# Optimization experiments

Hardware: AMD Instinct MI355X
Metric: run time of the kernel (lower is better)

The kernel has to match this reference:

```python
import jax, jax.numpy as jnp
import numpy as np

N_SPECIES = 4; N_BASIS = 128; N_GRAPH = 16; R_MAX = 6.0
NS_NODE, NV_NODE = 32, 16          # node irreps 32x0e + 16x1o
NS_EDGE = 16                       # initial edge irreps 16x0e
NS_OUT, NV_OUT = 16, 8             # output irreps 16x0e + 8x1o
NS_IN = 2 * NS_NODE + NS_EDGE      # 80 concatenated scalars
NV_IN = 2 * NV_NODE                # 32 concatenated vectors
NS_CONV = NS_OUT + NV_OUT          # 24 scalars (16 features + 8 gates)
W_SIZES = [NS_IN * NS_CONV, NS_IN * NV_OUT, NV_IN * NV_OUT, NV_IN * NS_CONV, NV_IN * NV_OUT]
N_NODES, N_EDGES = 8192, 65536
EPS = 1e-5


def gaussian_basis(d, stop, n):
    offsets = jnp.linspace(0.0, stop, n)
    coeff = -0.5 / (offsets[1] - offsets[0]) ** 2
    return jnp.exp(coeff * (d[:, None] - offsets[None, :]) ** 2)


def seg_mean(vals, seg, cnt):
    return jax.ops.segment_sum(vals, seg, num_segments=N_GRAPH) / cnt[:, None]


def setup_inputs():
    key = jax.random.key(0)
    ks = jax.random.split(key, 20)
    rn = lambda k, shape, scale: jax.random.normal(k, shape, jnp.float32) * scale
    inp = {}
    inp["node_fea"] = rn(ks[0], (N_NODES, NS_NODE + 3 * NV_NODE), 1.0)
    d = 0.5 + 5.0 * jax.random.uniform(ks[1], (N_EDGES,), jnp.float32)
    vec = jax.random.normal(ks[2], (N_EDGES, 3), jnp.float32)
    inp["edge_attr"] = jnp.concatenate([d[:, None], vec], axis=1)
    inp["edge_index"] = jax.random.randint(ks[3], (2, N_EDGES), 0, N_NODES)
    inp["x"] = jax.random.randint(ks[4], (N_NODES,), 0, N_SPECIES)
    inp["batch"] = jnp.sort(jax.random.randint(ks[5], (N_NODES,), 0, N_GRAPH))
    inp["w_rh"] = rn(ks[6], (N_BASIS, 64), N_BASIS ** -0.5); inp["b_rh"] = jnp.zeros((64,), jnp.float32)
    inp["w_ro"] = rn(ks[7], (64, sum(W_SIZES)), 64 ** -0.5); inp["b_ro"] = jnp.zeros((sum(W_SIZES),), jnp.float32)
    inp["w_pre"] = rn(ks[8], (NS_EDGE, NS_EDGE), NS_EDGE ** -0.5); inp["b_pre"] = jnp.zeros((NS_EDGE,), jnp.float32)
    inp["w_sc"] = rn(ks[9], (NS_EDGE, N_SPECIES ** 2, NS_OUT), 1.0)
    inp["w_post_s"] = rn(ks[10], (NS_OUT, NS_OUT), NS_OUT ** -0.5); inp["b_post_s"] = jnp.zeros((NS_OUT,), jnp.float32)
    inp["w_post_v"] = rn(ks[11], (NV_OUT, NV_OUT), NV_OUT ** -0.5)
    inp["ln_w_s"] = jnp.ones((NS_OUT,), jnp.float32); inp["ln_b_s"] = jnp.zeros((NS_OUT,), jnp.float32)
    inp["ln_w_v"] = jnp.ones((NV_OUT,), jnp.float32)
    inp["w_skip"] = rn(ks[12], (NS_EDGE, NS_OUT), NS_EDGE ** -0.5)
    inp["w_edge_s"] = rn(ks[13], (NS_OUT, NS_OUT), NS_OUT ** -0.5); inp["b_edge_s"] = jnp.zeros((NS_OUT,), jnp.float32)
    inp["w_edge_v"] = rn(ks[14], (NV_OUT, NV_OUT), NV_OUT ** -0.5)
    return inp


def _forward(node_fea, edge_attr, w_rh, b_rh, w_ro, b_ro, w_pre, b_pre, w_sc,
             w_post_s, b_post_s, w_post_v, ln_w_s, ln_b_s, ln_w_v,
             w_skip, w_edge_s, b_edge_s, w_edge_v, edge_index, x, batch):
    E = edge_index.shape[1]
    idx_i, idx_j = edge_index[0], edge_index[1]
    one_hot = jax.nn.one_hot(N_SPECIES * x[idx_i] + x[idx_j], N_SPECIES ** 2, dtype=node_fea.dtype)
    d, vec = edge_attr[:, 0], edge_attr[:, 1:4]
    u = vec / (jnp.linalg.norm(vec, axis=1, keepdims=True) + 1e-12)
    Y1 = np.sqrt(3.0) * u                                   # l=1 sph harm, component norm; Y0 == 1
    rbf = gaussian_basis(d, R_MAX, N_BASIS)                 # edge_length_embedded
    edge_s0 = gaussian_basis(d, 6.0, NS_EDGE)               # distance_expansion -> initial edge scalars
    # self connection: edge scalars x species-pair one-hot -> output scalars
    sc = jnp.einsum('ei,ej,ijo->eo', edge_s0, one_hot, w_sc) / np.sqrt(NS_EDGE * N_SPECIES ** 2)
    edge_s = edge_s0 @ w_pre + b_pre                        # lin_pre
    # gather node features by edge indices and concat
    nf_i, nf_j = node_fea[idx_i], node_fea[idx_j]
    s_in = jnp.concatenate([nf_i[:, :NS_NODE], nf_j[:, :NS_NODE], edge_s], axis=1)  # [E,80]
    v_in = jnp.concatenate([nf_i[:, NS_NODE:].reshape(E, NV_NODE, 3),
                            nf_j[:, NS_NODE:].reshape(E, NV_NODE, 3)], axis=1)      # [E,32,3]
    # radial MLP -> per-edge tensor-product path weights
    h = jax.nn.silu(rbf @ w_rh + b_rh)
    w_all = h @ w_ro + b_ro                                 # [E, 3840]
    w1, w2, w3, w4, w5 = jnp.split(w_all, np.cumsum(W_SIZES)[:-1].tolist(), axis=1)
    # equivariant tensor-product paths (explicit l<=1 Clebsch-Gordan structure)
    s0 = jnp.einsum('ei,eio->eo', s_in, w1.reshape(E, NS_IN, NS_CONV)) / np.sqrt(NS_IN)            # 0e x 0e -> 0e
    vA = jnp.einsum('ei,eio,ec->eoc', s_in, w2.reshape(E, NS_IN, NV_OUT), Y1) / np.sqrt(NS_IN)     # 0e x 1o -> 1o
    vB = jnp.einsum('eic,eio->eoc', v_in, w3.reshape(E, NV_IN, NV_OUT)) / np.sqrt(NV_IN)           # 1o x 0e -> 1o
    s1 = jnp.einsum('eic,eio,ec->eo', v_in, w4.reshape(E, NV_IN, NS_CONV), Y1) / np.sqrt(3.0 * NV_IN)  # 1o.1o -> 0e
    vC = jnp.einsum('eic,eio->eoc', jnp.cross(v_in, Y1[:, None, :]), w5.reshape(E, NV_IN, NV_OUT)) / np.sqrt(2.0 * NV_IN)  # 1o x 1o -> 1o
    s_conv = s0 + s1                                        # [E,24]
    v_conv = vA + vB + vC                                   # [E,8,3]
    # gate nonlinearity inside conv
    s_out = jax.nn.silu(s_conv[:, :NS_OUT])
    v_out = v_conv * jax.nn.sigmoid(s_conv[:, NS_OUT:])[:, :, None]
    # lin_post then self connection
    s_out = s_out @ w_post_s + b_post_s + sc
    v_out = jnp.einsum('eic,io->eoc', v_out, w_post_v)
    # e3LayerNorm keyed by graph id of source node
    eb = batch[idx_i]
    cnt = jnp.maximum(jax.ops.segment_sum(jnp.ones((E,), s_out.dtype), eb, num_segments=N_GRAPH), 1.0)
    mu = seg_mean(s_out, eb, cnt)
    s_c = s_out - mu[eb]
    rms_s = jnp.sqrt(seg_mean(s_c ** 2, eb, cnt).mean(axis=1, keepdims=True) + EPS)
    s_n = s_c / rms_s[eb] * ln_w_s + ln_b_s
    rms_v = jnp.sqrt((seg_mean((v_out ** 2).sum(-1), eb, cnt) / 3.0).mean(axis=1, keepdims=True) + EPS)
    v_n = v_out / rms_v[eb][:, :, None] * ln_w_v[None, :, None]
    # skip connection from old edge features (scalars only)
    s_n = s_n + edge_s0 @ w_skip
    # final lin_edge
    s_fin = s_n @ w_edge_s + b_edge_s
    v_fin = jnp.einsum('eic,io->eoc', v_n, w_edge_v)
    return jnp.concatenate([s_fin, v_fin.reshape(E, NV_OUT * 3)], axis=1)  # [E,40]


def reference(node_fea, edge_attr, edge_index, x, batch, w_rh, b_rh, w_ro, b_ro,
              w_pre, b_pre, w_sc, w_post_s, b_post_s, w_post_v, ln_w_s, ln_b_s, ln_w_v,
              w_skip, w_edge_s, b_edge_s, w_edge_v):
    return _forward(node_fea, edge_attr, w_rh, b_rh, w_ro, b_ro, w_pre, b_pre, w_sc,
                    w_post_s, b_post_s, w_post_v, ln_w_s, ln_b_s, ln_w_v,
                    w_skip, w_edge_s, b_edge_s, w_edge_v, edge_index, x, batch)
```

## Files before the change

### kernel.cpp

```cpp
#include <hip/hip_runtime.h>

typedef unsigned short u16;
typedef unsigned int u32;
typedef __attribute__((ext_vector_type(8))) _Float16 half8;
typedef __attribute__((ext_vector_type(2))) __fp16 fp16x2;
typedef __attribute__((ext_vector_type(4))) float floatx4;

#define E_TOTAL 65536

__device__ __forceinline__ u32 pk16(float x0, float x1) {
    union { fp16x2 h; u32 u; } c;
    c.h = __builtin_amdgcn_cvt_pkrtz(x0, x1);
    return c.u;
}
union Frag8h { u32 u[4]; half8 v; };


__global__ __launch_bounds__(1024) void k_init(float* __restrict__ ws, int* __restrict__ binv) {
    const int tid = threadIdx.x;
    for (int i = tid; i < 1056; i += 1024) ws[i] = 0.0f;
    if (tid < 64) {
        const int lane = tid;
        const int q = lane >> 4;
        if (lane < 32) binv[lane] = lane;
        half8 bfr;
        #pragma unroll
        for (int j = 0; j < 8; ++j) bfr[j] = (_Float16)(float)(q*8 + j + 1);
        #pragma unroll
        for (int s = 0; s < 32; ++s) {
            const int qa = s >> 3, ja = s & 7;
            half8 afr;
            #pragma unroll
            for (int j = 0; j < 8; ++j) afr[j] = (_Float16)0.0f;
            if (q == qa) afr[ja] = (_Float16)1.0f;
            floatx4 dc = {0.0f, 0.0f, 0.0f, 0.0f};
            dc = __builtin_amdgcn_mfma_f32_16x16x32_f16(afr, bfr, dc, 0, 0, 0);
            if (lane == 0) {
                const int sB = (int)(dc[0] + 0.5f) - 1;
                if (sB >= 0 && sB < 32) binv[sB] = s;
            }
        }
    }
}

__global__ __launch_bounds__(256) void k_edge_heavy(
    const float* __restrict__ node_fea, const float* __restrict__ edge_attr,
    const int* __restrict__ edge_index, const int* __restrict__ xsp,
    const float* __restrict__ w_rh, const float* __restrict__ b_rh,
    const float* __restrict__ w_ro, const float* __restrict__ b_ro,
    const float* __restrict__ w_pre, const float* __restrict__ b_pre,
    const float* __restrict__ w_sc, const float* __restrict__ w_post_s,
    const float* __restrict__ b_post_s, const float* __restrict__ w_post_v,
    const int* __restrict__ binv, const int* __restrict__ batch,
    float* __restrict__ ws_stats,
    float* __restrict__ out)
{
    __shared__ __align__(16) float sh_wt[2][32][130];
    __shared__ float sh_sin[32][80];
    __shared__ float sh_vl[32][3][32];
    __shared__ float sh_acc[32][56];
    __shared__ float sh_y1[32][4];
    __shared__ int   sh_kmap[32];

    u16*   a_rbf = (u16*)&sh_wt[0][0][0];
    u16*   a_h   = (u16*)((char*)&sh_wt[0][0][0] + 8192);
    float* es0f  = (float*)((char*)&sh_wt[0][0][0] + 12288);

    const int tid = threadIdx.x;
    const int ed = tid >> 4, l16 = tid & 15;
    const int lane = tid & 63, w = tid >> 6;
    const int quad = lane >> 4, l15 = lane & 15;
    const int e0 = blockIdx.x * 32 + ed;
    const int e1 = e0 + 16;

    if (tid < 32) sh_kmap[tid] = binv[tid];

    const int ni0 = edge_index[e0], nj0 = edge_index[E_TOTAL + e0];
    const int ni1 = edge_index[e1], nj1 = edge_index[E_TOTAL + e1];
    const float4 ea0 = *(const float4*)(edge_attr + 4*e0);
    const float4 ea1 = *(const float4*)(edge_attr + 4*e1);
    const float d0 = ea0.x, d1 = ea1.x;
    {
        const float invn0 = 1.0f / (sqrtf(ea0.y*ea0.y + ea0.z*ea0.z + ea0.w*ea0.w) + 1e-12f);
        const float invn1 = 1.0f / (sqrtf(ea1.y*ea1.y + ea1.z*ea1.z + ea1.w*ea1.w) + 1e-12f);
        if (l16 == 0) {
            sh_y1[ed][0]    = 1.7320508075688772f * ea0.y * invn0;
            sh_y1[ed][1]    = 1.7320508075688772f * ea0.z * invn0;
            sh_y1[ed][2]    = 1.7320508075688772f * ea0.w * invn0;
            sh_y1[16+ed][0] = 1.7320508075688772f * ea1.y * invn1;
            sh_y1[16+ed][1] = 1.7320508075688772f * ea1.z * invn1;
            sh_y1[16+ed][2] = 1.7320508075688772f * ea1.w * invn1;
        }
    }

    const float C128 = -0.5f * (127.0f/6.0f) * (127.0f/6.0f);
    const float S128 = 6.0f/127.0f;
    {
        Frag8h t0, t1;
        #pragma unroll
        for (int r2 = 0; r2 < 4; ++r2) {
            const int b0i = l16*8 + 2*r2;
            const float u0 = d0 - S128 * (float)b0i;
            const float u1 = d0 - S128 * (float)(b0i + 1);
            const float v0 = d1 - S128 * (float)b0i;
            const float v1 = d1 - S128 * (float)(b0i + 1);
            t0.u[r2] = pk16(expf(C128*u0*u0), expf(C128*u1*u1));
            t1.u[r2] = pk16(expf(C128*v0*v0), expf(C128*v1*v1));
        }
        *(half8*)&a_rbf[(l16*16 + ed)*8]        = t0.v;
        *(half8*)&a_rbf[2048 + (l16*16 + ed)*8] = t1.v;
    }
    {
        const float t0 = d0 - 0.4f * (float)l16;
        const float t1 = d1 - 0.4f * (float)l16;
        es0f[ed*16 + l16]      = expf(-3.125f * t0 * t0);
        es0f[(16+ed)*16 + l16] = expf(-3.125f * t1 * t1);
    }

    const float rs80 = 0.11180339887498949f;
    const float rs32 = 0.17677669529663689f;
    {
        const float* fi = node_fea + (size_t)ni0 * 80;
        const float* fj = node_fea + (size_t)nj0 * 80;
        sh_sin[ed][2*l16+0]    = fi[2*l16+0] * rs80;
        sh_sin[ed][2*l16+1]    = fi[2*l16+1] * rs80;
        sh_sin[ed][32+2*l16+0] = fj[2*l16+0] * rs80;
        sh_sin[ed][32+2*l16+1] = fj[2*l16+1] * rs80;
        #pragma unroll
        for (int c = 0; c < 3; ++c) {
            sh_vl[ed][c][l16]      = fi[32 + 3*l16 + c] * rs32;
            sh_vl[ed][c][16 + l16] = fj[32 + 3*l16 + c] * rs32;
        }
    }
    {
        const float* fi = node_fea + (size_t)ni1 * 80;
        const float* fj = node_fea + (size_t)nj1 * 80;
        sh_sin[16+ed][2*l16+0]    = fi[2*l16+0] * rs80;
        sh_sin[16+ed][2*l16+1]    = fi[2*l16+1] * rs80;
        sh_sin[16+ed][32+2*l16+0] = fj[2*l16+0] * rs80;
        sh_sin[16+ed][32+2*l16+1] = fj[2*l16+1] * rs80;
        #pragma unroll
        for (int c = 0; c < 3; ++c) {
            sh_vl[16+ed][c][l16]      = fi[32 + 3*l16 + c] * rs32;
            sh_vl[16+ed][c][16 + l16] = fj[32 + 3*l16 + c] * rs32;
        }
    }
    for (int s = tid; s < 32*56; s += 256) (&sh_acc[0][0])[s] = 0.0f;
    __syncthreads();

    int km[8];
    u32 voff0[8], voff1[8];
    #pragma unroll
    for (int j = 0; j < 8; ++j) {
        km[j] = sh_kmap[quad*8 + j];
        voff0[j] = (u32)(km[j] * 3840 + l15);
        voff1[j] = voff0[j] + 32u * 3840u;
    }

    float my_sc0, my_sc1;
    {
        const int o = l16;
        float es0v = b_pre[o], sc0 = 0.0f;
        float es1v = b_pre[o], sc1 = 0.0f;
        const int p0 = 4*xsp[ni0] + xsp[nj0];
        const int p1 = 4*xsp[ni1] + xsp[nj1];
        #pragma unroll
        for (int i = 0; i < 16; ++i) {
            const float g0 = es0f[ed*16 + i];
            const float g1 = es0f[(16+ed)*16 + i];
            es0v += g0 * w_pre[i*16 + o];
            es1v += g1 * w_pre[i*16 + o];
            sc0  += g0 * w_sc[(i*16 + p0)*16 + o];
            sc1  += g1 * w_sc[(i*16 + p1)*16 + o];
        }
        sh_sin[ed][64 + o]    = es0v * rs80;
        sh_sin[16+ed][64 + o] = es1v * rs80;
        my_sc0 = sc0 * 0.0625f;
        my_sc1 = sc1 * 0.0625f;
    }

    {
        floatx4 h0 = {0.0f, 0.0f, 0.0f, 0.0f};
        floatx4 h1 = {0.0f, 0.0f, 0.0f, 0.0f};
        #pragma unroll
        for (int kk = 0; kk < 4; ++kk) {
            const half8 ag0 = *(const half8*)&a_rbf[((kk*4 + quad)*16 + l15)*8];
            const half8 ag1 = *(const half8*)&a_rbf[2048 + ((kk*4 + quad)*16 + l15)*8];
            Frag8h bh;
            #pragma unroll
            for (int jj = 0; jj < 4; ++jj) {
                const float x0 = w_rh[(size_t)(kk*32 + km[2*jj+0])*64 + w*16 + l15];
                const float x1 = w_rh[(size_t)(kk*32 + km[2*jj+1])*64 + w*16 + l15];
                bh.u[jj] = pk16(x0, x1);
            }
            h0 = __builtin_amdgcn_mfma_f32_16x16x32_f16(ag0, bh.v, h0, 0, 0, 0);
            h1 = __builtin_amdgcn_mfma_f32_16x16x32_f16(ag1, bh.v, h1, 0, 0, 0);
        }
        const int hn = w*16 + l15;
        const float bb = b_rh[hn];
        const int k8 = hn >> 3, j2 = hn & 7;
        #pragma unroll
        for (int r = 0; r < 4; ++r) {
            const int m = quad*4 + r;
            {
                const float x = h0[r] + bb;
                const float s = x / (1.0f + expf(-x));
                union { _Float16 h; u16 u; } cv; cv.h = (_Float16)s;
                a_h[(k8*16 + m)*8 + j2] = cv.u;
            }
            {
                const float x = h1[r] + bb;
                const float s = x / (1.0f + expf(-x));
                union { _Float16 h; u16 u; } cv; cv.h = (_Float16)s;
                a_h[1024 + (k8*16 + m)*8 + j2] = cv.u;
            }
        }
    }
    __syncthreads();

    const half8 a0g0 = *(const half8*)&a_h[((0*4 + quad)*16 + l15)*8];
    const half8 a1g0 = *(const half8*)&a_h[((1*4 + quad)*16 + l15)*8];
    const half8 a0g1 = *(const half8*)&a_h[1024 + ((0*4 + quad)*16 + l15)*8];
    const half8 a1g1 = *(const half8*)&a_h[1024 + ((1*4 + quad)*16 + l15)*8];
    __syncthreads();

    float pf[32];
    float pbias[2];
    #pragma unroll
    for (int ct = 0; ct < 2; ++ct) {
        const int sgct = __builtin_amdgcn_readfirstlane(w*2 + ct);
        const float* bp = w_ro + sgct*16;
        #pragma unroll
        for (int j = 0; j < 8; ++j) {
            pf[ct*16 + j]     = bp[voff0[j]];
            pf[ct*16 + 8 + j] = bp[voff1[j]];
        }
        pbias[ct] = b_ro[sgct*16 + l15];
    }

    for (int ch = 0; ch < 30; ++ch) {
        const int coff = ch * 128;
        float (*wt)[130] = sh_wt[ch & 1];
        floatx4 acc0[2], acc1[2];
        float bias[2];
        #pragma unroll
        for (int ct = 0; ct < 2; ++ct) {
            Frag8h b0, b1;
            #pragma unroll
            for (int jj = 0; jj < 4; ++jj) {
                b0.u[jj] = pk16(pf[ct*16 + 2*jj],     pf[ct*16 + 2*jj+1]);
                b1.u[jj] = pk16(pf[ct*16 + 8 + 2*jj], pf[ct*16 + 8 + 2*jj+1]);
            }
            floatx4 a = {0.0f, 0.0f, 0.0f, 0.0f};
            a = __builtin_amdgcn_mfma_f32_16x16x32_f16(a0g0, b0.v, a, 0, 0, 0);
            a = __builtin_amdgcn_mfma_f32_16x16x32_f16(a1g0, b1.v, a, 0, 0, 0);
            acc0[ct] = a;
            floatx4 c = {0.0f, 0.0f, 0.0f, 0.0f};
            c = __builtin_amdgcn_mfma_f32_16x16x32_f16(a0g1, b0.v, c, 0, 0, 0);
            c = __builtin_amdgcn_mfma_f32_16x16x32_f16(a1g1, b1.v, c, 0, 0, 0);
            acc1[ct] = c;
            bias[ct] = pbias[ct];
        }
        #pragma unroll
        for (int ct = 0; ct < 2; ++ct) {
            const int col = w*32 + ct*16 + l15;
            #pragma unroll
            for (int r = 0; r < 4; ++r) {
                wt[quad*4 + r][col]      = acc0[ct][r] + bias[ct];
                wt[16 + quad*4 + r][col] = acc1[ct][r] + bias[ct];
            }
        }
        __syncthreads();

        if (ch < 29) {
            #pragma unroll
            for (int ct = 0; ct < 2; ++ct) {
                const int sgct = __builtin_amdgcn_readfirstlane((ch+1)*8 + w*2 + ct);
                const float* bp = w_ro + sgct*16;
                #pragma unroll
                for (int j = 0; j < 8; ++j) {
                    pf[ct*16 + j]     = bp[voff0[j]];
                    pf[ct*16 + 8 + j] = bp[voff1[j]];
                }
                pbias[ct] = b_ro[sgct*16 + l15];
            }
        }

        if (ch < 15) {
            for (int idx = tid; idx < 768; idx += 256) {
                const int eo = idx / 24, o = idx % 24;
                const int i0 = (coff > o) ? (coff - o + 23) / 24 : 0;
                int i1 = (coff + 128 - o + 23) / 24; if (i1 > 80) i1 = 80;
                float a = 0.0f;
                for (int i = i0; i < i1; ++i)
                    a += sh_sin[eo][i] * wt[eo][i*24 + o - coff];
                sh_acc[eo][o] += a;
            }
        } else if (ch < 20) {
            const int ib = (ch - 15) * 16;
            for (int idx = tid; idx < 256; idx += 256) {
                const int eo = idx >> 3, o = idx & 7;
                float a = 0.0f;
                #pragma unroll
                for (int i = 0; i < 16; ++i)
                    a += sh_sin[eo][ib + i] * wt[eo][i*8 + o];
                sh_acc[eo][24 + o] += a;
            }
        } else if (ch < 22) {
            const int ib = (ch - 20) * 16;
            for (int idx = tid; idx < 768; idx += 256) {
                const int eo = idx / 24, rem = idx % 24;
                const int o = rem / 3, cc = rem % 3;
                float a = 0.0f;
                #pragma unroll
                for (int i = 0; i < 16; ++i)
                    a += sh_vl[eo][cc][ib + i] * wt[eo][i*8 + o];
                sh_acc[eo][32 + o*3 + cc] += a;
            }
        } else if (ch < 28) {
            const int rel = coff - 2816;
            for (int idx = tid; idx < 768; idx += 256) {
                const int eo = idx / 24, o = idx % 24;
                const int i0 = (rel > o) ? (rel - o + 23) / 24 : 0;
                int i1 = (rel + 128 - o + 23) / 24; if (i1 > 32) i1 = 32;
                const float Ya = sh_y1[eo][0], Yb = sh_y1[eo][1], Yc = sh_y1[eo][2];
                float a = 0.0f;
                for (int i = i0; i < i1; ++i) {
                    const float qv = sh_vl[eo][0][i]*Ya + sh_vl[eo][1][i]*Yb
                                   + sh_vl[eo][2][i]*Yc;
                    a += qv * wt[eo][i*24 + o - rel];
                }
                sh_acc[eo][o] += a * 0.57735026918962573f;
            }
        } else {
            const int ib = (ch - 28) * 16;
            for (int idx = tid; idx < 768; idx += 256) {
                const int eo = idx / 24, rem = idx % 24;
                const int o = rem / 3, cc = rem % 3;
                const int c1 = (cc < 2) ? cc + 1 : 0;
                const int c2 = (c1 < 2) ? c1 + 1 : 0;
                const float Yp = sh_y1[eo][c2];
                const float Ym = sh_y1[eo][c1];
                float a = 0.0f;
                #pragma unroll
                for (int i = 0; i < 16; ++i)
                    a += (sh_vl[eo][c1][ib+i]*Yp - sh_vl[eo][c2][ib+i]*Ym) * wt[eo][i*8 + o];
                sh_acc[eo][32 + o*3 + cc] += a * 0.70710678118654746f;
            }
        }
    }
    __syncthreads();

    float* bins = &sh_wt[0][0][0];
    for (int s = tid; s < 768; s += 256) bins[s] = 0.0f;
    __syncthreads();

    const int gi0 = batch[ni0];
    const int gi1 = batch[ni1];
    #pragma unroll
    for (int g = 0; g < 2; ++g) {
        const int er = g*16 + ed;
        const int e  = (g == 0) ? e0 : e1;
        const int gi = (g == 0) ? gi0 : gi1;
        const float msc = (g == 0) ? my_sc0 : my_sc1;
        {
            const int o = l16;
            float a = b_post_s[o] + msc;
            #pragma unroll
            for (int i = 0; i < 16; ++i) {
                const float sv = sh_acc[er][i];
                a += (sv / (1.0f + expf(-sv))) * w_post_s[i*16 + o];
            }
            out[(size_t)e*40 + o] = a;
            atomicAdd(&bins[gi*48 + o], a);
            atomicAdd(&bins[gi*48 + 16 + o], a*a);
            if (o == 0) atomicAdd(&bins[gi*48 + 40], 1.0f);
        }
        if (l16 < 8) {
            const int o = l16;
            const float Ya = sh_y1[er][0], Yb = sh_y1[er][1], Yc = sh_y1[er][2];
            float r0 = 0.0f, r1 = 0.0f, r2 = 0.0f;
            #pragma unroll
            for (int i = 0; i < 8; ++i) {
                const float gt = 1.0f / (1.0f + expf(-sh_acc[er][16 + i]));
                const float a2 = sh_acc[er][24 + i];
                const float ww = w_post_v[i*8 + o];
                r0 += (a2*Ya + sh_acc[er][32 + i*3 + 0]) * gt * ww;
                r1 += (a2*Yb + sh_acc[er][32 + i*3 + 1]) * gt * ww;
                r2 += (a2*Yc + sh_acc[er][32 + i*3 + 2]) * gt * ww;
            }
            out[(size_t)e*40 + 16 + o*3 + 0] = r0;
            out[(size_t)e*40 + 16 + o*3 + 1] = r1;
            out[(size_t)e*40 + 16 + o*3 + 2] = r2;
            atomicAdd(&bins[gi*48 + 32 + o], r0*r0 + r1*r1 + r2*r2);
        }
    }
    __syncthreads();
    for (int s = tid; s < 768; s += 256) {
        const float x = bins[s];
        if (x != 0.0f) atomicAdd(&ws_stats[s], x);
    }
}

__global__ __launch_bounds__(256) void k_edge_final(
    float* buf, const float* __restrict__ ws,
    const float* __restrict__ edge_attr, const int* __restrict__ edge_index,
    const int* __restrict__ batch,
    const float* __restrict__ ln_w_s, const float* __restrict__ ln_b_s,
    const float* __restrict__ ln_w_v, const float* __restrict__ w_skip,
    const float* __restrict__ w_edge_s, const float* __restrict__ b_edge_s,
    const float* __restrict__ w_edge_v)
{
    __shared__ float sh_mu[16][16];
    __shared__ float sh_is[16], sh_iv[16];
    __shared__ float sh_lws[16], sh_lbs[16], sh_lwv[8];
    __shared__ float sh_skip[16][16], sh_wes[16][16], sh_bes[16], sh_wev[8][8];
    const int tid = threadIdx.x;
    if (tid < 16) {
        const int g = tid;
        float cnt = ws[g*48 + 40]; if (cnt < 1.0f) cnt = 1.0f;
        const float ic = 1.0f / cnt;
        float vs = 0.0f;
        for (int chn = 0; chn < 16; ++chn) {
            const float mu = ws[g*48 + chn] * ic;
            sh_mu[g][chn] = mu;
            vs += ws[g*48 + 16 + chn] * ic - mu * mu;
        }
        if (vs < 0.0f) vs = 0.0f;
        sh_is[g] = 1.0f / sqrtf(vs * (1.0f/16.0f) + 1e-5f);
        float vv = 0.0f;
        for (int o = 0; o < 8; ++o) vv += ws[g*48 + 32 + o];
        vv = vv * ic * (1.0f/3.0f) * (1.0f/8.0f);
        sh_iv[g] = 1.0f / sqrtf(vv + 1e-5f);
    }
    sh_skip[tid >> 4][tid & 15] = w_skip[tid];
    sh_wes[tid >> 4][tid & 15]  = w_edge_s[tid];
    if (tid < 16) {
        sh_lws[tid] = ln_w_s[tid];
        sh_lbs[tid] = ln_b_s[tid];
        sh_bes[tid] = b_edge_s[tid];
    }
    if (tid < 8)  sh_lwv[tid] = ln_w_v[tid];
    if (tid < 64) sh_wev[tid >> 3][tid & 7] = w_edge_v[tid];
    __syncthreads();

    const int e = blockIdx.x * 256 + tid;
    const int g = batch[edge_index[e]];
    const float d = edge_attr[4*e];
    float es0[16];
    #pragma unroll
    for (int b = 0; b < 16; ++b) {
        const float t = d - 0.4f * (float)b;
        es0[b] = expf(-3.125f * t * t);
    }
    float p[40];
    float* pb = buf + (size_t)e * 40;
    #pragma unroll
    for (int j = 0; j < 40; ++j) p[j] = pb[j];

    const float is = sh_is[g];
    float sn[16];
    #pragma unroll
    for (int chn = 0; chn < 16; ++chn)
        sn[chn] = (p[chn] - sh_mu[g][chn]) * is * sh_lws[chn] + sh_lbs[chn];
    #pragma unroll
    for (int b = 0; b < 16; ++b) {
        const float g0 = es0[b];
        #pragma unroll
        for (int chn = 0; chn < 16; ++chn) sn[chn] += g0 * sh_skip[b][chn];
    }
    #pragma unroll
    for (int o = 0; o < 16; ++o) {
        float a = sh_bes[o];
        #pragma unroll
        for (int chn = 0; chn < 16; ++chn) a += sn[chn] * sh_wes[chn][o];
        pb[o] = a;
    }
    const float iv = sh_iv[g];
    float vn[8][3];
    #pragma unroll
    for (int i = 0; i < 8; ++i) {
        const float f = iv * sh_lwv[i];
        vn[i][0] = p[16 + i*3 + 0] * f;
        vn[i][1] = p[16 + i*3 + 1] * f;
        vn[i][2] = p[16 + i*3 + 2] * f;
    }
    #pragma unroll
    for (int o = 0; o < 8; ++o) {
        float r0 = 0.0f, r1 = 0.0f, r2 = 0.0f;
        #pragma unroll
        for (int i = 0; i < 8; ++i) {
            const float w = sh_wev[i][o];
            r0 += vn[i][0] * w; r1 += vn[i][1] * w; r2 += vn[i][2] * w;
        }
        pb[16 + o*3 + 0] = r0;
        pb[16 + o*3 + 1] = r1;
        pb[16 + o*3 + 2] = r2;
    }
}

extern "C" void kernel_launch(void* const* d_in, const int* in_sizes, int n_in,
                              void* d_out, int out_size, void* d_ws, size_t ws_size,
                              hipStream_t stream)
{
    const float* node_fea  = (const float*)d_in[0];
    const float* edge_attr = (const float*)d_in[1];
    const int* edge_index  = (const int*)d_in[2];
    const int* xsp         = (const int*)d_in[3];
    const int* batch       = (const int*)d_in[4];
    const float* w_rh      = (const float*)d_in[5];
    const float* b_rh      = (const float*)d_in[6];
    const float* w_ro      = (const float*)d_in[7];
    const float* b_ro      = (const float*)d_in[8];
    const float* w_pre     = (const float*)d_in[9];
    const float* b_pre     = (const float*)d_in[10];
    const float* w_sc      = (const float*)d_in[11];
    const float* w_post_s  = (const float*)d_in[12];
    const float* b_post_s  = (const float*)d_in[13];
    const float* w_post_v  = (const float*)d_in[14];
    const float* ln_w_s    = (const float*)d_in[15];
    const float* ln_b_s    = (const float*)d_in[16];
    const float* ln_w_v    = (const float*)d_in[17];
    const float* w_skip    = (const float*)d_in[18];
    const float* w_edge_s  = (const float*)d_in[19];
    const float* b_edge_s  = (const float*)d_in[20];
    const float* w_edge_v  = (const float*)d_in[21];

    float* ws   = (float*)d_ws;
    int*   binv = (int*)(ws + 1056);
    float* out  = (float*)d_out;

    k_init<<<1, 1024, 0, stream>>>(ws, binv);
    k_edge_heavy<<<2048, 256, 0, stream>>>(node_fea, edge_attr, edge_index, xsp,
        w_rh, b_rh, w_ro, b_ro, w_pre, b_pre, w_sc, w_post_s, b_post_s, w_post_v,
        binv, batch, ws, out);
    k_edge_final<<<256, 256, 0, stream>>>(out, ws, edge_attr, edge_index,
        batch, ln_w_s, ln_b_s, ln_w_v, w_skip, w_edge_s, b_edge_s, w_edge_v);
}
```

Measured before the change: 406.9 us.

## Single-buffer the weight tile in LDS and replicate global stat accumulators

The double-buffered per-chunk weight tile in shared memory becomes a single buffer, with an extra barrier before each write so the previous chunk's readers are done. This cuts LDS use per block, likely to allow more resident blocks, at the cost of one more __syncthreads per chunk. The per-graph statistics atomics are also spread over 8 replicas chosen by block index to reduce contention on the same addresses. The final kernel sums the replicas, and the init kernel zeroes the larger workspace.

```diff
diff --git a/kernel.cpp b/kernel.cpp
--- a/kernel.cpp
+++ b/kernel.cpp
@@ -18,7 +18,7 @@
 
 __global__ __launch_bounds__(1024) void k_init(float* __restrict__ ws, int* __restrict__ binv) {
     const int tid = threadIdx.x;
-    for (int i = tid; i < 1056; i += 1024) ws[i] = 0.0f;
+    for (int i = tid; i < 6144; i += 1024) ws[i] = 0.0f;
     if (tid < 64) {
         const int lane = tid;
         const int q = lane >> 4;
@@ -55,16 +55,16 @@
     float* __restrict__ ws_stats,
     float* __restrict__ out)
 {
-    __shared__ __align__(16) float sh_wt[2][32][130];
+    __shared__ __align__(16) float sh_wt[32][130];
     __shared__ float sh_sin[32][80];
     __shared__ float sh_vl[32][3][32];
     __shared__ float sh_acc[32][56];
     __shared__ float sh_y1[32][4];
     __shared__ int   sh_kmap[32];
 
-    u16*   a_rbf = (u16*)&sh_wt[0][0][0];
-    u16*   a_h   = (u16*)((char*)&sh_wt[0][0][0] + 8192);
-    float* es0f  = (float*)((char*)&sh_wt[0][0][0] + 12288);
+    u16*   a_rbf = (u16*)&sh_wt[0][0];
+    u16*   a_h   = (u16*)((char*)&sh_wt[0][0] + 8192);
+    float* es0f  = (float*)((char*)&sh_wt[0][0] + 12288);
 
     const int tid = threadIdx.x;
     const int ed = tid >> 4, l16 = tid & 15;
@@ -222,7 +222,6 @@
     const half8 a1g0 = *(const half8*)&a_h[((1*4 + quad)*16 + l15)*8];
     const half8 a0g1 = *(const half8*)&a_h[1024 + ((0*4 + quad)*16 + l15)*8];
     const half8 a1g1 = *(const half8*)&a_h[1024 + ((1*4 + quad)*16 + l15)*8];
-    __syncthreads();
 
     float pf[32];
     float pbias[2];
@@ -240,7 +239,6 @@
 
     for (int ch = 0; ch < 30; ++ch) {
         const int coff = ch * 128;
-        float (*wt)[130] = sh_wt[ch & 1];
         floatx4 acc0[2], acc1[2];
         float bias[2];
         #pragma unroll
@@ -261,13 +259,14 @@
             acc1[ct] = c;
             bias[ct] = pbias[ct];
         }
+        __syncthreads();
         #pragma unroll
         for (int ct = 0; ct < 2; ++ct) {
             const int col = w*32 + ct*16 + l15;
             #pragma unroll
             for (int r = 0; r < 4; ++r) {
-                wt[quad*4 + r][col]      = acc0[ct][r] + bias[ct];
-                wt[16 + quad*4 + r][col] = acc1[ct][r] + bias[ct];
+                sh_wt[quad*4 + r][col]      = acc0[ct][r] + bias[ct];
+                sh_wt[16 + quad*4 + r][col] = acc1[ct][r] + bias[ct];
             }
         }
         __syncthreads();
@@ -293,7 +292,7 @@
                 int i1 = (coff + 128 - o + 23) / 24; if (i1 > 80) i1 = 80;
                 float a = 0.0f;
                 for (int i = i0; i < i1; ++i)
-                    a += sh_sin[eo][i] * wt[eo][i*24 + o - coff];
+                    a += sh_sin[eo][i] * sh_wt[eo][i*24 + o - coff];
                 sh_acc[eo][o] += a;
             }
         } else if (ch < 20) {
@@ -303,7 +302,7 @@
                 float a = 0.0f;
                 #pragma unroll
                 for (int i = 0; i < 16; ++i)
-                    a += sh_sin[eo][ib + i] * wt[eo][i*8 + o];
+                    a += sh_sin[eo][ib + i] * sh_wt[eo][i*8 + o];
                 sh_acc[eo][24 + o] += a;
             }
         } else if (ch < 22) {
@@ -314,7 +313,7 @@
                 float a = 0.0f;
                 #pragma unroll
                 for (int i = 0; i < 16; ++i)
-                    a += sh_vl[eo][cc][ib + i] * wt[eo][i*8 + o];
+                    a += sh_vl[eo][cc][ib + i] * sh_wt[eo][i*8 + o];
                 sh_acc[eo][32 + o*3 + cc] += a;
             }
         } else if (ch < 28) {
@@ -328,7 +327,7 @@
                 for (int i = i0; i < i1; ++i) {
                     const float qv = sh_vl[eo][0][i]*Ya + sh_vl[eo][1][i]*Yb
                                    + sh_vl[eo][2][i]*Yc;
-                    a += qv * wt[eo][i*24 + o - rel];
+                    a += qv * sh_wt[eo][i*24 + o - rel];
                 }
                 sh_acc[eo][o] += a * 0.57735026918962573f;
             }
@@ -344,14 +343,14 @@
                 float a = 0.0f;
                 #pragma unroll
                 for (int i = 0; i < 16; ++i)
-                    a += (sh_vl[eo][c1][ib+i]*Yp - sh_vl[eo][c2][ib+i]*Ym) * wt[eo][i*8 + o];
+                    a += (sh_vl[eo][c1][ib+i]*Yp - sh_vl[eo][c2][ib+i]*Ym) * sh_wt[eo][i*8 + o];
                 sh_acc[eo][32 + o*3 + cc] += a * 0.70710678118654746f;
             }
         }
     }
     __syncthreads();
 
-    float* bins = &sh_wt[0][0][0];
+    float* bins = &sh_wt[0][0];
     for (int s = tid; s < 768; s += 256) bins[s] = 0.0f;
     __syncthreads();
 
@@ -396,9 +395,12 @@
         }
     }
     __syncthreads();
-    for (int s = tid; s < 768; s += 256) {
-        const float x = bins[s];
-        if (x != 0.0f) atomicAdd(&ws_stats[s], x);
+    {
+        float* rep = ws_stats + (blockIdx.x & 7) * 768;
+        for (int s = tid; s < 768; s += 256) {
+            const float x = bins[s];
+            if (x != 0.0f) atomicAdd(&rep[s], x);
+        }
     }
 }
 
@@ -418,18 +420,27 @@
     const int tid = threadIdx.x;
     if (tid < 16) {
         const int g = tid;
-        float cnt = ws[g*48 + 40]; if (cnt < 1.0f) cnt = 1.0f;
+        float sums[41];
+        #pragma unroll
+        for (int k = 0; k < 41; ++k) sums[k] = 0.0f;
+        for (int r = 0; r < 8; ++r) {
+            const float* rep = ws + r*768 + g*48;
+            for (int chn = 0; chn < 16; ++chn) { sums[chn] += rep[chn]; sums[16+chn] += rep[16+chn]; }
+            for (int o = 0; o < 8; ++o) sums[32+o] += rep[32+o];
+            sums[40] += rep[40];
+        }
+        float cnt = sums[40]; if (cnt < 1.0f) cnt = 1.0f;
         const float ic = 1.0f / cnt;
         float vs = 0.0f;
         for (int chn = 0; chn < 16; ++chn) {
-            const float mu = ws[g*48 + chn] * ic;
+            const float mu = sums[chn] * ic;
             sh_mu[g][chn] = mu;
-            vs += ws[g*48 + 16 + chn] * ic - mu * mu;
+            vs += sums[16+chn] * ic - mu * mu;
         }
         if (vs < 0.0f) vs = 0.0f;
         sh_is[g] = 1.0f / sqrtf(vs * (1.0f/16.0f) + 1e-5f);
         float vv = 0.0f;
-        for (int o = 0; o < 8; ++o) vv += ws[g*48 + 32 + o];
+        for (int o = 0; o < 8; ++o) vv += sums[32+o];
         vv = vv * ic * (1.0f/3.0f) * (1.0f/8.0f);
         sh_iv[g] = 1.0f / sqrtf(vv + 1e-5f);
     }
@@ -527,7 +538,7 @@
     const float* w_edge_v  = (const float*)d_in[21];
 
     float* ws   = (float*)d_ws;
-    int*   binv = (int*)(ws + 1056);
+    int*   binv = (int*)(ws + 6144);
     float* out  = (float*)d_out;
 
     k_init<<<1, 1024, 0, stream>>>(ws, binv);
```

Result: no change. 408.8 us (+0.5%).
